# Kernel tuning notes

Hardware: AMD Instinct MI355X
Metric: run time of the kernel (lower is better)

The kernel has to match this reference:

```python
import jax, jax.numpy as jnp
import numpy as np

SPOT_DIM = 512
PROTEIN_DIM = 512
NUM_CLASSES = 32
NUM_PROTEINS = 64
BATCH = 4096
INPUT_DIM = SPOT_DIM + NUM_CLASSES          # 544
H1 = INPUT_DIM // 4                          # 136
H2 = INPUT_DIM // 2                          # 272


def leaky_relu(x, slope=0.2):
    return jnp.where(x > 0, x, slope * x)


def setup_inputs() -> dict:
    key = jax.random.key(0)
    ks = jax.random.split(key, 13)
    s = 0.02
    return {
        "cell_embeddings_protein": jax.random.normal(ks[0], (BATCH, SPOT_DIM), jnp.float32),
        "cond_label": jax.random.normal(ks[1], (BATCH, NUM_CLASSES), jnp.float32),
        "protein_emb": jax.random.normal(ks[2], (BATCH, NUM_PROTEINS, PROTEIN_DIM), jnp.float32),
        # protein_projection: Linear(protein_dim -> spot_dim)
        "proj_W": jax.random.normal(ks[3], (PROTEIN_DIM, SPOT_DIM), jnp.float32) * s,
        "proj_b": jnp.zeros((SPOT_DIM,), jnp.float32),
        # trans_dim: Linear(input_dim + spot_dim -> input_dim)
        "trans_W": jax.random.normal(ks[4], (INPUT_DIM + SPOT_DIM, INPUT_DIM), jnp.float32) * s,
        "trans_b": jnp.zeros((INPUT_DIM,), jnp.float32),
        # per-protein 3-layer MLPs, stacked over proteins (grouped GEMM form)
        "W1": jax.random.normal(ks[5], (NUM_PROTEINS, INPUT_DIM, H1), jnp.float32) * s,
        "b1": jnp.zeros((NUM_PROTEINS, H1), jnp.float32),
        "W2": jax.random.normal(ks[6], (NUM_PROTEINS, H1, H2), jnp.float32) * s,
        "b2": jnp.zeros((NUM_PROTEINS, H2), jnp.float32),
        "W3": jax.random.normal(ks[7], (NUM_PROTEINS, H2, 1), jnp.float32) * s,
        "b3": jnp.zeros((NUM_PROTEINS, 1), jnp.float32),
    }


def reference(cell_embeddings_protein, cond_label, protein_emb,
              proj_W, proj_b, trans_W, trans_b,
              W1, b1, W2, b2, W3, b3):
    # [B, P, spot_dim]
    protein_projected = jnp.einsum("bpd,de->bpe", protein_emb, proj_W) + proj_b
    # [B, input_dim] -> broadcast to [B, P, input_dim]
    spot_encoded = jnp.concatenate([cell_embeddings_protein, cond_label], axis=-1)
    spot_encoded = jnp.broadcast_to(spot_encoded[:, None, :],
                                    (spot_encoded.shape[0], NUM_PROTEINS, INPUT_DIM))
    x = jnp.concatenate([protein_projected, spot_encoded], axis=-1)  # [B,P,1056]
    x = jnp.einsum("bpi,io->bpo", x, trans_W) + trans_b              # [B,P,544]
    # grouped per-protein MLP as batched matmuls over P
    h = leaky_relu(jnp.einsum("bpi,pij->bpj", x, W1) + b1)           # [B,P,136]
    h = leaky_relu(jnp.einsum("bpj,pjk->bpk", h, W2) + b2)           # [B,P,272]
    out = jnp.einsum("bpk,pko->bpo", h, W3) + b3                     # [B,P,1]
    return out[..., 0]                                               # [B,P]
```

## Files before the change

kernel.cpp:

```cpp
#include <hip/hip_runtime.h>


typedef short bf16x8 __attribute__((ext_vector_type(8)));
typedef unsigned short u16;
typedef u16 u16x8 __attribute__((ext_vector_type(8)));
typedef float f32x4 __attribute__((ext_vector_type(4)));

typedef const void __attribute__((address_space(1)))* gas_p;
typedef void __attribute__((address_space(3)))* las_p;

__device__ __forceinline__ void gl_lds16(const void* g, void* l) {
  __builtin_amdgcn_global_load_lds((gas_p)g, (las_p)l, 16, 0, 0);
}

__device__ __forceinline__ u16 f2bf(float f) {
  union { float f; unsigned u; } x; x.f = f;
  return (u16)((x.u + 0x7FFFu + ((x.u >> 16) & 1u)) >> 16);
}


__global__ __launch_bounds__(256)
void k_g(const float* __restrict__ projW, const float* __restrict__ transW,
         float* __restrict__ G) {
  __shared__ float As[16][68];
  __shared__ float Bs[16][68];
  const int t = threadIdx.x;
  const int m0 = blockIdx.x * 64, c0 = blockIdx.y * 64;
  const int tx = t & 15, ty = t >> 4;
  const int ar = t >> 2, akk = (t & 3) * 4;
  const int bkk = t >> 4, bcc = (t & 15) * 4;
  const bool bok = (c0 + bcc) < 544;
  float acc[4][4];
#pragma unroll
  for (int i = 0; i < 4; ++i)
#pragma unroll
    for (int j = 0; j < 4; ++j) acc[i][j] = 0.f;

  for (int k0 = 0; k0 < 512; k0 += 16) {
    const float4 av = *(const float4*)(projW + (size_t)(m0 + ar) * 512 + k0 + akk);
    float4 bv = {0.f, 0.f, 0.f, 0.f};
    if (bok) bv = *(const float4*)(transW + (size_t)(k0 + bkk) * 544 + c0 + bcc);
    __syncthreads();
    As[akk + 0][ar] = av.x; As[akk + 1][ar] = av.y;
    As[akk + 2][ar] = av.z; As[akk + 3][ar] = av.w;
    *(float4*)&Bs[bkk][bcc] = bv;
    __syncthreads();
#pragma unroll
    for (int kk = 0; kk < 16; ++kk) {
      const float4 a = *(const float4*)&As[kk][ty * 4];
      const float4 b = *(const float4*)&Bs[kk][tx * 4];
      const float aa[4] = {a.x, a.y, a.z, a.w};
      const float bb[4] = {b.x, b.y, b.z, b.w};
#pragma unroll
      for (int i = 0; i < 4; ++i)
#pragma unroll
        for (int j = 0; j < 4; ++j) acc[i][j] += aa[i] * bb[j];
    }
  }
  if ((c0 + tx * 4) < 544) {
#pragma unroll
    for (int i = 0; i < 4; ++i) {
      float4 v = {acc[i][0], acc[i][1], acc[i][2], acc[i][3]};
      *(float4*)(G + (size_t)(m0 + ty * 4 + i) * 544 + c0 + tx * 4) = v;
    }
  }
}

__global__ void k_gcopy(const float* __restrict__ transW, float* __restrict__ G) {
  const int idx = blockIdx.x * 256 + threadIdx.x;
  if (idx >= 73984) return;
  ((float4*)G)[69632 + idx] = ((const float4*)transW)[69632 + idx];
}

__global__ void k_d(const float* __restrict__ projb, const float* __restrict__ transW,
                    const float* __restrict__ transb, float* __restrict__ dvec) {
  __shared__ float red[256];
  const int t = threadIdx.x;
  const int c = blockIdx.x * 32 + (t & 31);
  const int kp = t >> 5;
  float s = 0.f;
  for (int k = kp * 64; k < kp * 64 + 64; ++k) s += projb[k] * transW[(size_t)k * 544 + c];
  red[t] = s;
  __syncthreads();
  if (t < 32) {
    float v = red[t];
#pragma unroll
    for (int j = 1; j < 8; ++j) v += red[t + 32 * j];
    dvec[blockIdx.x * 32 + t] = v + transb[blockIdx.x * 32 + t];
  }
}

__global__ void k_c(const float* __restrict__ dvec, const float* __restrict__ W1,
                    const float* __restrict__ b1, float* __restrict__ cvec) {
  __shared__ float red[256];
  const int t = threadIdx.x;
  const int p = blockIdx.x, cg = blockIdx.y;
  const int col = cg * 16 + (t & 15);
  const int kp = t >> 4;
  float s = 0.f;
  if (col < 136) {
    const float* w = W1 + (size_t)p * 544 * 136;
    for (int k = kp * 34; k < kp * 34 + 34; ++k) s += dvec[k] * w[(size_t)k * 136 + col];
  }
  red[t] = s;
  __syncthreads();
  if (t < 16) {
    float v = 0.f;
#pragma unroll
    for (int j = 0; j < 16; ++j) v += red[j * 16 + t];
    const int c2 = cg * 16 + t;
    cvec[p * 144 + c2] = (c2 < 136) ? v + b1[p * 136 + c2] : 0.f;
  }
}

__global__ void k_pack_w1(const float* __restrict__ W1, u16* __restrict__ W1pk) {
  const int uid = blockIdx.x * 256 + threadIdx.x;
  const int unit = uid & 63;
  const int rest = uid >> 6;
  const int n = rest % 9;
  const int tile = rest / 9;
  const int kt = tile % 17;
  const int pp = tile / 17;
  const int kb = unit >> 4, cl = unit & 15;
  const int colg = n * 16 + cl;
  u16x8 v;
#pragma unroll
  for (int j = 0; j < 8; ++j) {
    const int k = kt * 32 + kb * 8 + j;
    v[j] = (colg < 136) ? f2bf(W1[((size_t)pp * 544 + k) * 136 + colg]) : (u16)0;
  }
  *(u16x8*)(W1pk + (size_t)uid * 8) = v;
}

__global__ void k_pack_w2(const float* __restrict__ W2, u16* __restrict__ W2pk) {
  const int uid = blockIdx.x * 256 + threadIdx.x;
  const int unit = uid & 63;
  const int rest = uid >> 6;
  const int n = rest % 17;
  const int tile = rest / 17;
  const int kt = tile % 5;
  const int pp = tile / 5;
  const int kb = unit >> 4, cl = unit & 15;
  const int colg = n * 16 + cl;
  u16x8 v;
#pragma unroll
  for (int j = 0; j < 8; ++j) {
    const int k = kt * 32 + kb * 8 + j;
    v[j] = (k < 136) ? f2bf(W2[((size_t)pp * 136 + k) * 272 + colg]) : (u16)0;
  }
  *(u16x8*)(W2pk + (size_t)uid * 8) = v;
}

__global__ __launch_bounds__(256, 2)
void k_pk3(const float* __restrict__ G, const u16* __restrict__ W1pk,
           u16* __restrict__ Wpk) {
  __shared__ char smem[34816];
  char* const Ab0 = smem;
  char* const Bb0 = smem + 16384;
  const int t = threadIdx.x, lane = t & 63, w = t >> 6;
  const int l15 = lane & 15, kq = lane >> 4;
  const int mt = blockIdx.x, p = blockIdx.y;
  const int sr = t >> 1, sh = t & 1, sf = (sr >> 1) & 3;
  const int gr = mt * 128 + sr;
  const bool aval = (gr < 1056);

  const f32x4 fz = {0.f, 0.f, 0.f, 0.f};
  f32x4 acc[2][9];
#pragma unroll
  for (int m = 0; m < 2; ++m)
#pragma unroll
    for (int n = 0; n < 9; ++n) acc[m][n] = fz;

  const u16* wsrc = W1pk + (size_t)p * (17 * 4608);

  float4 pv[4];
  auto preloadA = [&](int kt) {
    if (aval) {
      const float* s = G + (size_t)gr * 544 + kt * 32 + sh * 16;
#pragma unroll
      for (int j = 0; j < 4; ++j) pv[j] = *(const float4*)(s + j * 4);
    } else {
      const float4 z4 = {0.f, 0.f, 0.f, 0.f};
#pragma unroll
      for (int j = 0; j < 4; ++j) pv[j] = z4;
    }
  };
  auto writeA = [&](int buf) {
    u16x8 v0, v1;
    v0[0] = f2bf(pv[0].x); v0[1] = f2bf(pv[0].y); v0[2] = f2bf(pv[0].z); v0[3] = f2bf(pv[0].w);
    v0[4] = f2bf(pv[1].x); v0[5] = f2bf(pv[1].y); v0[6] = f2bf(pv[1].z); v0[7] = f2bf(pv[1].w);
    v1[0] = f2bf(pv[2].x); v1[1] = f2bf(pv[2].y); v1[2] = f2bf(pv[2].z); v1[3] = f2bf(pv[2].w);
    v1[4] = f2bf(pv[3].x); v1[5] = f2bf(pv[3].y); v1[6] = f2bf(pv[3].z); v1[7] = f2bf(pv[3].w);
    char* dst = Ab0 + buf * 8192 + sr * 64;
    *(u16x8*)(dst + ((((sh << 1)) ^ sf) << 4)) = v0;
    *(u16x8*)(dst + ((((sh << 1) | 1) ^ sf) << 4)) = v1;
  };
  auto stageB = [&](int kt, int buf) {
    const u16* src = wsrc + kt * 4608;
    char* dst = Bb0 + buf * 9216;
    for (int i = w; i < 9; i += 4) gl_lds16(src + i * 512 + lane * 8, dst + i * 1024);
  };
  auto compute = [&](int buf) {
    const char* A = Ab0 + buf * 8192;
    const char* Bt = Bb0 + buf * 9216;
    bf16x8 a[2];
#pragma unroll
    for (int m = 0; m < 2; ++m) {
      const int row = w * 32 + m * 16 + l15;
      a[m] = *(const bf16x8*)(A + row * 64 + ((kq ^ ((row >> 1) & 3)) << 4));
    }
#pragma unroll
    for (int n = 0; n < 9; ++n) {
      bf16x8 b = *(const bf16x8*)(Bt + n * 1024 + lane * 16);
      acc[0][n] = __builtin_amdgcn_mfma_f32_16x16x32_bf16(a[0], b, acc[0][n], 0, 0, 0);
      acc[1][n] = __builtin_amdgcn_mfma_f32_16x16x32_bf16(a[1], b, acc[1][n], 0, 0, 0);
    }
  };

  preloadA(0); stageB(0, 0); writeA(0);
  for (int kt = 0; kt < 17; ++kt) {
    __syncthreads();
    const int buf = kt & 1;
    if (kt + 1 < 17) { preloadA(kt + 1); stageB(kt + 1, buf ^ 1); }
    compute(buf);
    if (kt + 1 < 17) writeA(buf ^ 1);
  }

#pragma unroll
  for (int m = 0; m < 2; ++m)
#pragma unroll
    for (int n = 0; n < 9; ++n)
#pragma unroll
      for (int i = 0; i < 4; ++i) {
        const int row = mt * 128 + w * 32 + m * 16 + (kq << 2) + i;
        if (row < 1056) {
          const int ktw = row >> 5, kk = row & 31;
          const size_t off = (size_t)(p * 33 + ktw) * 4608 + n * 512 +
                             ((kk >> 3) * 16 + l15) * 8 + (kk & 7);
          Wpk[off] = f2bf(acc[m][n][i]);
        }
      }
}

__global__ __launch_bounds__(256, 2)
void k_main(const float* __restrict__ cell, const float* __restrict__ cond,
            const float* __restrict__ pe,
            const u16* __restrict__ Wpk, const u16* __restrict__ W2pk,
            const float* __restrict__ cvec, const float* __restrict__ b2,
            const float* __restrict__ W3, const float* __restrict__ b3,
            float* __restrict__ out) {
  __shared__ char smem[58368];
  char* const Ab0 = smem;
  char* const Bb0 = smem + 16384;
  char* const h1  = smem + 17408;
  char* const B2  = smem;

  const int t = threadIdx.x, lane = t & 63, w = t >> 6;
  const int l15 = lane & 15, kq = lane >> 4;
  const int p = blockIdx.y;
  const int b0 = blockIdx.x * 128;
  const int sr = t >> 1, sh = t & 1, sf = (sr >> 1) & 3;
  const long gr = b0 + sr;

  const f32x4 fz = {0.f, 0.f, 0.f, 0.f};
  f32x4 acc[2][9];
#pragma unroll
  for (int m = 0; m < 2; ++m)
#pragma unroll
    for (int n = 0; n < 9; ++n) acc[m][n] = fz;

  const u16* wsrc = Wpk + (size_t)p * (33 * 4608);

  float4 pv[4];
  auto preloadA = [&](int kt) {
    const float* s;
    if (kt < 16)      s = pe + ((gr * 64 + p) << 9) + kt * 32 + sh * 16;
    else if (kt < 32) s = cell + (gr << 9) + (kt - 16) * 32 + sh * 16;
    else              s = cond + (gr << 5) + sh * 16;
#pragma unroll
    for (int j = 0; j < 4; ++j) pv[j] = *(const float4*)(s + j * 4);
  };
  auto writeA = [&](int buf) {
    u16x8 v0, v1;
    v0[0] = f2bf(pv[0].x); v0[1] = f2bf(pv[0].y); v0[2] = f2bf(pv[0].z); v0[3] = f2bf(pv[0].w);
    v0[4] = f2bf(pv[1].x); v0[5] = f2bf(pv[1].y); v0[6] = f2bf(pv[1].z); v0[7] = f2bf(pv[1].w);
    v1[0] = f2bf(pv[2].x); v1[1] = f2bf(pv[2].y); v1[2] = f2bf(pv[2].z); v1[3] = f2bf(pv[2].w);
    v1[4] = f2bf(pv[3].x); v1[5] = f2bf(pv[3].y); v1[6] = f2bf(pv[3].z); v1[7] = f2bf(pv[3].w);
    char* dst = Ab0 + buf * 8192 + sr * 64;
    *(u16x8*)(dst + ((((sh << 1)) ^ sf) << 4)) = v0;
    *(u16x8*)(dst + ((((sh << 1) | 1) ^ sf) << 4)) = v1;
  };
  auto stageB = [&](int kt, int buf) {
    const u16* src = wsrc + kt * 4608;
    char* dst = Bb0 + buf * 9216;
    for (int i = w; i < 9; i += 4) gl_lds16(src + i * 512 + lane * 8, dst + i * 1024);
  };
  auto compute1 = [&](int buf) {
    const char* A = Ab0 + buf * 8192;
    const char* Bt = Bb0 + buf * 9216;
    bf16x8 a[2];
#pragma unroll
    for (int m = 0; m < 2; ++m) {
      const int row = w * 32 + m * 16 + l15;
      a[m] = *(const bf16x8*)(A + row * 64 + ((kq ^ ((row >> 1) & 3)) << 4));
    }
#pragma unroll
    for (int n = 0; n < 9; ++n) {
      bf16x8 b = *(const bf16x8*)(Bt + n * 1024 + lane * 16);
      acc[0][n] = __builtin_amdgcn_mfma_f32_16x16x32_bf16(a[0], b, acc[0][n], 0, 0, 0);
      acc[1][n] = __builtin_amdgcn_mfma_f32_16x16x32_bf16(a[1], b, acc[1][n], 0, 0, 0);
    }
  };

  preloadA(0); stageB(0, 0); writeA(0);
  for (int kt = 0; kt < 33; ++kt) {
    __syncthreads();
    const int buf = kt & 1;
    if (kt + 1 < 33) { preloadA(kt + 1); stageB(kt + 1, buf ^ 1); }
    compute1(buf);
    if (kt + 1 < 33) writeA(buf ^ 1);
  }
  __syncthreads();

  {
    const float* cp = cvec + p * 144;
#pragma unroll
    for (int m = 0; m < 2; ++m) {
      const int rb = w * 32 + m * 16 + (kq << 2);
#pragma unroll
      for (int n = 0; n < 9; ++n) {
        const int col = n * 16 + l15;
        const float cb = cp[col];
#pragma unroll
        for (int i = 0; i < 4; ++i) {
          const int row = rb + i;
          float v = acc[m][n][i] + cb;
          v = v > 0.f ? v : 0.2f * v;
          const int u = (col >> 3) ^ ((row >> 1) & 3);
          *(u16*)(h1 + row * 320 + u * 16 + ((col & 7) << 1)) = f2bf(v);
        }
      }
    }
    const int uz = (18 + sh) ^ sf;
    u16x8 z = {0, 0, 0, 0, 0, 0, 0, 0};
    *(u16x8*)(h1 + sr * 320 + uz * 16) = z;
  }

  f32x4 acc2[2][17];
#pragma unroll
  for (int m = 0; m < 2; ++m)
#pragma unroll
    for (int n = 0; n < 17; ++n) acc2[m][n] = fz;

  const u16* w2src = W2pk + (size_t)p * (5 * 8704);
  for (int kt = 0; kt < 5; ++kt) {
    for (int i = w; i < 17; i += 4)
      gl_lds16(w2src + kt * 8704 + i * 512 + lane * 8, B2 + i * 1024);
    __syncthreads();
    bf16x8 a[2];
#pragma unroll
    for (int m = 0; m < 2; ++m) {
      const int row = w * 32 + m * 16 + l15;
      const int u = (kt * 4 + kq) ^ ((row >> 1) & 3);
      a[m] = *(const bf16x8*)(h1 + row * 320 + u * 16);
    }
#pragma unroll
    for (int n = 0; n < 17; ++n) {
      bf16x8 b = *(const bf16x8*)(B2 + n * 1024 + lane * 16);
      acc2[0][n] = __builtin_amdgcn_mfma_f32_16x16x32_bf16(a[0], b, acc2[0][n], 0, 0, 0);
      acc2[1][n] = __builtin_amdgcn_mfma_f32_16x16x32_bf16(a[1], b, acc2[1][n], 0, 0, 0);
    }
    __syncthreads();
  }

  {
    const float* w3p = W3 + p * 272;
    const float* b2p = b2 + p * 272;
    const float b3v = b3[p];
    float w3v[17], b2v[17];
#pragma unroll
    for (int n = 0; n < 17; ++n) { w3v[n] = w3p[n * 16 + l15]; b2v[n] = b2p[n * 16 + l15]; }
#pragma unroll
    for (int m = 0; m < 2; ++m) {
#pragma unroll
      for (int i = 0; i < 4; ++i) {
        float s = 0.f;
#pragma unroll
        for (int n = 0; n < 17; ++n) {
          float h = acc2[m][n][i] + b2v[n];
          h = h > 0.f ? h : 0.2f * h;
          s += h * w3v[n];
        }
        s += __shfl_xor(s, 1);
        s += __shfl_xor(s, 2);
        s += __shfl_xor(s, 4);
        s += __shfl_xor(s, 8);
        if (l15 == 0) {
          const int row = w * 32 + m * 16 + (kq << 2) + i;
          out[(size_t)(b0 + row) * 64 + p] = s + b3v;
        }
      }
    }
  }
}

extern "C" void kernel_launch(void* const* d_in, const int* in_sizes, int n_in,
                              void* d_out, int out_size, void* d_ws, size_t ws_size,
                              hipStream_t stream) {
  const float* cell   = (const float*)d_in[0];
  const float* cond   = (const float*)d_in[1];
  const float* pe     = (const float*)d_in[2];
  const float* projW  = (const float*)d_in[3];
  const float* projb  = (const float*)d_in[4];
  const float* transW = (const float*)d_in[5];
  const float* transb = (const float*)d_in[6];
  const float* W1     = (const float*)d_in[7];
  const float* b1     = (const float*)d_in[8];
  const float* W2     = (const float*)d_in[9];
  const float* b2     = (const float*)d_in[10];
  const float* W3     = (const float*)d_in[11];
  const float* b3     = (const float*)d_in[12];
  float* out = (float*)d_out;

  char* ws = (char*)d_ws;
  float* G    = (float*)(ws);
  u16*  W1pk  = (u16*)(ws + 2297856);
  u16*  Wpk   = (u16*)(ws + 12324864);
  u16*  W2pk  = (u16*)(ws + 31789056);
  float* dvec = (float*)(ws + 37359616);
  float* cvec = (float*)(ws + 37361792);

  k_g      <<<dim3(8, 9),   256, 0, stream>>>(projW, transW, G);
  k_gcopy  <<<289,  256, 0, stream>>>(transW, G);
  k_d      <<<17,   256, 0, stream>>>(projb, transW, transb, dvec);
  k_c      <<<dim3(64, 9),  256, 0, stream>>>(dvec, W1, b1, cvec);
  k_pack_w1<<<2448, 256, 0, stream>>>(W1, W1pk);
  k_pack_w2<<<1360, 256, 0, stream>>>(W2, W2pk);
  k_pk3    <<<dim3(9, 64),  256, 0, stream>>>(G, W1pk, Wpk);
  k_main   <<<dim3(32, 64), 256, 0, stream>>>(cell, cond, pe, Wpk, W2pk, cvec, b2, W3, b3, out);
}
```

Baseline: 328.9 us.

## Merge preprocessing kernels, fold bias GEMV into pk3, retile main to 2x2 waves

Six small preprocessing launches become one k_pre kernel that dispatches on block index. The bias vector d is written as an extra row of G, so k_pk3 produces cvec as a byproduct and k_d and k_c go away. Both MFMA kernels change their wave tiling from 4x1 to 2x2, giving each wave 64 rows by up to 5 column tiles to raise A and B register reuse. k_main also gets a swizzled 1D block-to-protein mapping for cache locality and a larger LDS layout. The larger LDS footprint and accumulator count may lower occupancy.

```diff
diff --git a/kernel.cpp b/kernel.cpp
--- a/kernel.cpp
+++ b/kernel.cpp
@@ -18,172 +18,146 @@
   return (u16)((x.u + 0x7FFFu + ((x.u >> 16) & 1u)) >> 16);
 }
 
-
 __global__ __launch_bounds__(256)
-void k_g(const float* __restrict__ projW, const float* __restrict__ transW,
-         float* __restrict__ G) {
+void k_pre(const float* __restrict__ projW, const float* __restrict__ transW,
+           const float* __restrict__ projb, const float* __restrict__ transb,
+           const float* __restrict__ W1, const float* __restrict__ W2,
+           float* __restrict__ G, u16* __restrict__ W1pk, u16* __restrict__ W2pk) {
   __shared__ float As[16][68];
   __shared__ float Bs[16][68];
-  const int t = threadIdx.x;
-  const int m0 = blockIdx.x * 64, c0 = blockIdx.y * 64;
-  const int tx = t & 15, ty = t >> 4;
-  const int ar = t >> 2, akk = (t & 3) * 4;
-  const int bkk = t >> 4, bcc = (t & 15) * 4;
-  const bool bok = (c0 + bcc) < 544;
-  float acc[4][4];
-#pragma unroll
-  for (int i = 0; i < 4; ++i)
-#pragma unroll
-    for (int j = 0; j < 4; ++j) acc[i][j] = 0.f;
-
-  for (int k0 = 0; k0 < 512; k0 += 16) {
-    const float4 av = *(const float4*)(projW + (size_t)(m0 + ar) * 512 + k0 + akk);
-    float4 bv = {0.f, 0.f, 0.f, 0.f};
-    if (bok) bv = *(const float4*)(transW + (size_t)(k0 + bkk) * 544 + c0 + bcc);
+  const int bb = blockIdx.x, t = threadIdx.x;
+
+  if (bb < 72) {
+    const int m0 = (bb & 7) * 64, c0 = (bb >> 3) * 64;
+    const int tx = t & 15, ty = t >> 4;
+    const int ar = t >> 2, akk = (t & 3) * 4;
+    const int bkk = t >> 4, bcc = (t & 15) * 4;
+    const bool bok = (c0 + bcc) < 544;
+    float acc[4][4];
+#pragma unroll
+    for (int i = 0; i < 4; ++i)
+#pragma unroll
+      for (int j = 0; j < 4; ++j) acc[i][j] = 0.f;
+    for (int k0 = 0; k0 < 512; k0 += 16) {
+      const float4 av = *(const float4*)(projW + (size_t)(m0 + ar) * 512 + k0 + akk);
+      float4 bv = {0.f, 0.f, 0.f, 0.f};
+      if (bok) bv = *(const float4*)(transW + (size_t)(k0 + bkk) * 544 + c0 + bcc);
+      __syncthreads();
+      As[akk + 0][ar] = av.x; As[akk + 1][ar] = av.y;
+      As[akk + 2][ar] = av.z; As[akk + 3][ar] = av.w;
+      *(float4*)&Bs[bkk][bcc] = bv;
+      __syncthreads();
+#pragma unroll
+      for (int kk = 0; kk < 16; ++kk) {
+        const float4 a = *(const float4*)&As[kk][ty * 4];
+        const float4 b = *(const float4*)&Bs[kk][tx * 4];
+        const float aa[4] = {a.x, a.y, a.z, a.w};
+        const float bb2[4] = {b.x, b.y, b.z, b.w};
+#pragma unroll
+        for (int i = 0; i < 4; ++i)
+#pragma unroll
+          for (int j = 0; j < 4; ++j) acc[i][j] += aa[i] * bb2[j];
+      }
+    }
+    if ((c0 + tx * 4) < 544) {
+#pragma unroll
+      for (int i = 0; i < 4; ++i) {
+        float4 v = {acc[i][0], acc[i][1], acc[i][2], acc[i][3]};
+        *(float4*)(G + (size_t)(m0 + ty * 4 + i) * 544 + c0 + tx * 4) = v;
+      }
+    }
+  } else if (bb < 361) {
+    const int idx = (bb - 72) * 256 + t;
+    if (idx < 73984) ((float4*)G)[69632 + idx] = ((const float4*)transW)[69632 + idx];
+  } else if (bb < 378) {
+    __shared__ float red[256];
+    const int c = (bb - 361) * 32 + (t & 31);
+    const int kp = t >> 5;
+    float s = 0.f;
+    for (int k = kp * 64; k < kp * 64 + 64; ++k) s += projb[k] * transW[(size_t)k * 544 + c];
+    red[t] = s;
     __syncthreads();
-    As[akk + 0][ar] = av.x; As[akk + 1][ar] = av.y;
-    As[akk + 2][ar] = av.z; As[akk + 3][ar] = av.w;
-    *(float4*)&Bs[bkk][bcc] = bv;
-    __syncthreads();
-#pragma unroll
-    for (int kk = 0; kk < 16; ++kk) {
-      const float4 a = *(const float4*)&As[kk][ty * 4];
-      const float4 b = *(const float4*)&Bs[kk][tx * 4];
-      const float aa[4] = {a.x, a.y, a.z, a.w};
-      const float bb[4] = {b.x, b.y, b.z, b.w};
-#pragma unroll
-      for (int i = 0; i < 4; ++i)
-#pragma unroll
-        for (int j = 0; j < 4; ++j) acc[i][j] += aa[i] * bb[j];
-    }
-  }
-  if ((c0 + tx * 4) < 544) {
-#pragma unroll
-    for (int i = 0; i < 4; ++i) {
-      float4 v = {acc[i][0], acc[i][1], acc[i][2], acc[i][3]};
-      *(float4*)(G + (size_t)(m0 + ty * 4 + i) * 544 + c0 + tx * 4) = v;
-    }
-  }
-}
-
-__global__ void k_gcopy(const float* __restrict__ transW, float* __restrict__ G) {
-  const int idx = blockIdx.x * 256 + threadIdx.x;
-  if (idx >= 73984) return;
-  ((float4*)G)[69632 + idx] = ((const float4*)transW)[69632 + idx];
-}
-
-__global__ void k_d(const float* __restrict__ projb, const float* __restrict__ transW,
-                    const float* __restrict__ transb, float* __restrict__ dvec) {
-  __shared__ float red[256];
-  const int t = threadIdx.x;
-  const int c = blockIdx.x * 32 + (t & 31);
-  const int kp = t >> 5;
-  float s = 0.f;
-  for (int k = kp * 64; k < kp * 64 + 64; ++k) s += projb[k] * transW[(size_t)k * 544 + c];
-  red[t] = s;
-  __syncthreads();
-  if (t < 32) {
-    float v = red[t];
-#pragma unroll
-    for (int j = 1; j < 8; ++j) v += red[t + 32 * j];
-    dvec[blockIdx.x * 32 + t] = v + transb[blockIdx.x * 32 + t];
-  }
-}
-
-__global__ void k_c(const float* __restrict__ dvec, const float* __restrict__ W1,
-                    const float* __restrict__ b1, float* __restrict__ cvec) {
-  __shared__ float red[256];
-  const int t = threadIdx.x;
-  const int p = blockIdx.x, cg = blockIdx.y;
-  const int col = cg * 16 + (t & 15);
-  const int kp = t >> 4;
-  float s = 0.f;
-  if (col < 136) {
-    const float* w = W1 + (size_t)p * 544 * 136;
-    for (int k = kp * 34; k < kp * 34 + 34; ++k) s += dvec[k] * w[(size_t)k * 136 + col];
-  }
-  red[t] = s;
-  __syncthreads();
-  if (t < 16) {
-    float v = 0.f;
-#pragma unroll
-    for (int j = 0; j < 16; ++j) v += red[j * 16 + t];
-    const int c2 = cg * 16 + t;
-    cvec[p * 144 + c2] = (c2 < 136) ? v + b1[p * 136 + c2] : 0.f;
-  }
-}
-
-__global__ void k_pack_w1(const float* __restrict__ W1, u16* __restrict__ W1pk) {
-  const int uid = blockIdx.x * 256 + threadIdx.x;
-  const int unit = uid & 63;
-  const int rest = uid >> 6;
-  const int n = rest % 9;
-  const int tile = rest / 9;
-  const int kt = tile % 17;
-  const int pp = tile / 17;
-  const int kb = unit >> 4, cl = unit & 15;
-  const int colg = n * 16 + cl;
-  u16x8 v;
-#pragma unroll
-  for (int j = 0; j < 8; ++j) {
-    const int k = kt * 32 + kb * 8 + j;
-    v[j] = (colg < 136) ? f2bf(W1[((size_t)pp * 544 + k) * 136 + colg]) : (u16)0;
-  }
-  *(u16x8*)(W1pk + (size_t)uid * 8) = v;
-}
-
-__global__ void k_pack_w2(const float* __restrict__ W2, u16* __restrict__ W2pk) {
-  const int uid = blockIdx.x * 256 + threadIdx.x;
-  const int unit = uid & 63;
-  const int rest = uid >> 6;
-  const int n = rest % 17;
-  const int tile = rest / 17;
-  const int kt = tile % 5;
-  const int pp = tile / 5;
-  const int kb = unit >> 4, cl = unit & 15;
-  const int colg = n * 16 + cl;
-  u16x8 v;
-#pragma unroll
-  for (int j = 0; j < 8; ++j) {
-    const int k = kt * 32 + kb * 8 + j;
-    v[j] = (k < 136) ? f2bf(W2[((size_t)pp * 136 + k) * 272 + colg]) : (u16)0;
-  }
-  *(u16x8*)(W2pk + (size_t)uid * 8) = v;
+    if (t < 32) {
+      float v = red[t];
+#pragma unroll
+      for (int j = 1; j < 8; ++j) v += red[t + 32 * j];
+      const int cc = (bb - 361) * 32 + t;
+      G[(size_t)1056 * 544 + cc] = v + transb[cc];
+    }
+  } else if (bb < 391) {
+    const int idx = (bb - 378) * 256 + t;
+    const float4 z = {0.f, 0.f, 0.f, 0.f};
+#pragma unroll
+    for (int j = 0; j < 4; ++j) {
+      const int k = idx + j * 3328;
+      if (k < 12920) ((float4*)G)[143752 + k] = z;
+    }
+  } else if (bb < 2839) {
+    const int uid = (bb - 391) * 256 + t;
+    const int unit = uid & 63;
+    const int rest = uid >> 6;
+    const int n = rest % 9;
+    const int tile = rest / 9;
+    const int kt = tile % 17;
+    const int pp = tile / 17;
+    const int kb = unit >> 4, cl = unit & 15;
+    const int colg = n * 16 + cl;
+    u16x8 v;
+#pragma unroll
+    for (int j = 0; j < 8; ++j) {
+      const int k = kt * 32 + kb * 8 + j;
+      v[j] = (colg < 136) ? f2bf(W1[((size_t)pp * 544 + k) * 136 + colg]) : (u16)0;
+    }
+    *(u16x8*)(W1pk + (size_t)uid * 8) = v;
+  } else {
+    const int uid = (bb - 2839) * 256 + t;
+    const int unit = uid & 63;
+    const int rest = uid >> 6;
+    const int n = rest % 17;
+    const int tile = rest / 17;
+    const int kt = tile % 5;
+    const int pp = tile / 5;
+    const int kb = unit >> 4, cl = unit & 15;
+    const int colg = n * 16 + cl;
+    u16x8 v;
+#pragma unroll
+    for (int j = 0; j < 8; ++j) {
+      const int k = kt * 32 + kb * 8 + j;
+      v[j] = (k < 136) ? f2bf(W2[((size_t)pp * 136 + k) * 272 + colg]) : (u16)0;
+    }
+    *(u16x8*)(W2pk + (size_t)uid * 8) = v;
+  }
 }
 
 __global__ __launch_bounds__(256, 2)
 void k_pk3(const float* __restrict__ G, const u16* __restrict__ W1pk,
-           u16* __restrict__ Wpk) {
+           const float* __restrict__ b1, u16* __restrict__ Wpk,
+           float* __restrict__ cvec) {
   __shared__ char smem[34816];
   char* const Ab0 = smem;
   char* const Bb0 = smem + 16384;
   const int t = threadIdx.x, lane = t & 63, w = t >> 6;
   const int l15 = lane & 15, kq = lane >> 4;
+  const int mg = w >> 1, ng = w & 1;
+  const int n0 = ng * 5, nn = ng ? 4 : 5;
   const int mt = blockIdx.x, p = blockIdx.y;
   const int sr = t >> 1, sh = t & 1, sf = (sr >> 1) & 3;
   const int gr = mt * 128 + sr;
-  const bool aval = (gr < 1056);
 
   const f32x4 fz = {0.f, 0.f, 0.f, 0.f};
-  f32x4 acc[2][9];
-#pragma unroll
-  for (int m = 0; m < 2; ++m)
-#pragma unroll
-    for (int n = 0; n < 9; ++n) acc[m][n] = fz;
+  f32x4 acc[4][5];
+#pragma unroll
+  for (int m = 0; m < 4; ++m)
+#pragma unroll
+    for (int n = 0; n < 5; ++n) acc[m][n] = fz;
 
   const u16* wsrc = W1pk + (size_t)p * (17 * 4608);
 
   float4 pv[4];
   auto preloadA = [&](int kt) {
-    if (aval) {
-      const float* s = G + (size_t)gr * 544 + kt * 32 + sh * 16;
-#pragma unroll
-      for (int j = 0; j < 4; ++j) pv[j] = *(const float4*)(s + j * 4);
-    } else {
-      const float4 z4 = {0.f, 0.f, 0.f, 0.f};
-#pragma unroll
-      for (int j = 0; j < 4; ++j) pv[j] = z4;
-    }
+    const float* s = G + (size_t)gr * 544 + kt * 32 + sh * 16;
+#pragma unroll
+    for (int j = 0; j < 4; ++j) pv[j] = *(const float4*)(s + j * 4);
   };
   auto writeA = [&](int buf) {
     u16x8 v0, v1;
@@ -203,17 +177,20 @@
   auto compute = [&](int buf) {
     const char* A = Ab0 + buf * 8192;
     const char* Bt = Bb0 + buf * 9216;
-    bf16x8 a[2];
-#pragma unroll
-    for (int m = 0; m < 2; ++m) {
-      const int row = w * 32 + m * 16 + l15;
+    bf16x8 a[4];
+#pragma unroll
+    for (int m = 0; m < 4; ++m) {
+      const int row = mg * 64 + m * 16 + l15;
       a[m] = *(const bf16x8*)(A + row * 64 + ((kq ^ ((row >> 1) & 3)) << 4));
     }
 #pragma unroll
-    for (int n = 0; n < 9; ++n) {
-      bf16x8 b = *(const bf16x8*)(Bt + n * 1024 + lane * 16);
-      acc[0][n] = __builtin_amdgcn_mfma_f32_16x16x32_bf16(a[0], b, acc[0][n], 0, 0, 0);
-      acc[1][n] = __builtin_amdgcn_mfma_f32_16x16x32_bf16(a[1], b, acc[1][n], 0, 0, 0);
+    for (int n = 0; n < 5; ++n) {
+      if (n < nn) {
+        bf16x8 b = *(const bf16x8*)(Bt + (n0 + n) * 1024 + lane * 16);
+#pragma unroll
+        for (int m = 0; m < 4; ++m)
+          acc[m][n] = __builtin_amdgcn_mfma_f32_16x16x32_bf16(a[m], b, acc[m][n], 0, 0, 0);
+      }
     }
   };
 
@@ -227,19 +204,25 @@
   }
 
 #pragma unroll
-  for (int m = 0; m < 2; ++m)
-#pragma unroll
-    for (int n = 0; n < 9; ++n)
-#pragma unroll
-      for (int i = 0; i < 4; ++i) {
-        const int row = mt * 128 + w * 32 + m * 16 + (kq << 2) + i;
-        if (row < 1056) {
-          const int ktw = row >> 5, kk = row & 31;
-          const size_t off = (size_t)(p * 33 + ktw) * 4608 + n * 512 +
-                             ((kk >> 3) * 16 + l15) * 8 + (kk & 7);
-          Wpk[off] = f2bf(acc[m][n][i]);
+  for (int m = 0; m < 4; ++m)
+#pragma unroll
+    for (int n = 0; n < 5; ++n) {
+      if (n < nn) {
+#pragma unroll
+        for (int i = 0; i < 4; ++i) {
+          const int row = mt * 128 + mg * 64 + m * 16 + (kq << 2) + i;
+          const int col = (n0 + n) * 16 + l15;
+          if (row < 1056) {
+            const int ktw = row >> 5, kk = row & 31;
+            const size_t off = (size_t)(p * 33 + ktw) * 4608 + (n0 + n) * 512 +
+                               ((kk >> 3) * 16 + l15) * 8 + (kk & 7);
+            Wpk[off] = f2bf(acc[m][n][i]);
+          } else if (row == 1056) {
+            cvec[p * 144 + col] = (col < 136) ? acc[m][n][i] + b1[p * 136 + col] : 0.f;
+          }
         }
       }
+    }
 }
 
 __global__ __launch_bounds__(256, 2)
@@ -249,25 +232,30 @@
             const float* __restrict__ cvec, const float* __restrict__ b2,
             const float* __restrict__ W3, const float* __restrict__ b3,
             float* __restrict__ out) {
-  __shared__ char smem[58368];
-  char* const Ab0 = smem;
-  char* const Bb0 = smem + 16384;
-  char* const h1  = smem + 17408;
-  char* const B2  = smem;
+  __shared__ char smem[75776];
+  char* const h1  = smem;
+  char* const Ab0 = smem + 40960;
+  char* const Bb0 = smem + 57344;
+  char* const B2  = smem + 40960;
 
   const int t = threadIdx.x, lane = t & 63, w = t >> 6;
   const int l15 = lane & 15, kq = lane >> 4;
-  const int p = blockIdx.y;
-  const int b0 = blockIdx.x * 128;
+  const int mg = w >> 1, ng = w & 1;
+  const int n0 = ng * 5, nn = ng ? 4 : 5;
+
+  const unsigned lid = blockIdx.x;
+  const int p  = ((lid & 7) << 3) | ((lid >> 8) & 7);
+  const int b0 = ((lid >> 3) & 31) * 128;
+
   const int sr = t >> 1, sh = t & 1, sf = (sr >> 1) & 3;
   const long gr = b0 + sr;
 
   const f32x4 fz = {0.f, 0.f, 0.f, 0.f};
-  f32x4 acc[2][9];
-#pragma unroll
-  for (int m = 0; m < 2; ++m)
-#pragma unroll
-    for (int n = 0; n < 9; ++n) acc[m][n] = fz;
+  f32x4 acc[4][5];
+#pragma unroll
+  for (int m = 0; m < 4; ++m)
+#pragma unroll
+    for (int n = 0; n < 5; ++n) acc[m][n] = fz;
 
   const u16* wsrc = Wpk + (size_t)p * (33 * 4608);
 
@@ -298,17 +286,20 @@
   auto compute1 = [&](int buf) {
     const char* A = Ab0 + buf * 8192;
     const char* Bt = Bb0 + buf * 9216;
-    bf16x8 a[2];
-#pragma unroll
-    for (int m = 0; m < 2; ++m) {
-      const int row = w * 32 + m * 16 + l15;
+    bf16x8 a[4];
+#pragma unroll
+    for (int m = 0; m < 4; ++m) {
+      const int row = mg * 64 + m * 16 + l15;
       a[m] = *(const bf16x8*)(A + row * 64 + ((kq ^ ((row >> 1) & 3)) << 4));
     }
 #pragma unroll
-    for (int n = 0; n < 9; ++n) {
-      bf16x8 b = *(const bf16x8*)(Bt + n * 1024 + lane * 16);
-      acc[0][n] = __builtin_amdgcn_mfma_f32_16x16x32_bf16(a[0], b, acc[0][n], 0, 0, 0);
-      acc[1][n] = __builtin_amdgcn_mfma_f32_16x16x32_bf16(a[1], b, acc[1][n], 0, 0, 0);
+    for (int n = 0; n < 5; ++n) {
+      if (n < nn) {
+        bf16x8 b = *(const bf16x8*)(Bt + (n0 + n) * 1024 + lane * 16);
+#pragma unroll
+        for (int m = 0; m < 4; ++m)
+          acc[m][n] = __builtin_amdgcn_mfma_f32_16x16x32_bf16(a[m], b, acc[m][n], 0, 0, 0);
+      }
     }
   };
 
@@ -325,19 +316,21 @@
   {
     const float* cp = cvec + p * 144;
 #pragma unroll
-    for (int m = 0; m < 2; ++m) {
-      const int rb = w * 32 + m * 16 + (kq << 2);
-#pragma unroll
-      for (int n = 0; n < 9; ++n) {
-        const int col = n * 16 + l15;
-        const float cb = cp[col];
-#pragma unroll
-        for (int i = 0; i < 4; ++i) {
-          const int row = rb + i;
-          float v = acc[m][n][i] + cb;
-          v = v > 0.f ? v : 0.2f * v;
-          const int u = (col >> 3) ^ ((row >> 1) & 3);
-          *(u16*)(h1 + row * 320 + u * 16 + ((col & 7) << 1)) = f2bf(v);
+    for (int m = 0; m < 4; ++m) {
+      const int rb = mg * 64 + m * 16 + (kq << 2);
+#pragma unroll
+      for (int n = 0; n < 5; ++n) {
+        if (n < nn) {
+          const int col = (n0 + n) * 16 + l15;
+          const float cb = cp[col];
+#pragma unroll
+          for (int i = 0; i < 4; ++i) {
+            const int row = rb + i;
+            float v = acc[m][n][i] + cb;
+            v = v > 0.f ? v : 0.2f * v;
+            const int u = (col >> 3) ^ ((row >> 1) & 3);
+            *(u16*)(h1 + row * 320 + u * 16 + ((col & 7) << 1)) = f2bf(v);
+          }
         }
       }
     }
@@ -345,6 +338,7 @@
     u16x8 z = {0, 0, 0, 0, 0, 0, 0, 0};
     *(u16x8*)(h1 + sr * 320 + uz * 16) = z;
   }
+  __syncthreads();
 
   f32x4 acc2[2][17];
 #pragma unroll
@@ -424,18 +418,12 @@
 
   char* ws = (char*)d_ws;
   float* G    = (float*)(ws);
-  u16*  W1pk  = (u16*)(ws + 2297856);
-  u16*  Wpk   = (u16*)(ws + 12324864);
-  u16*  W2pk  = (u16*)(ws + 31789056);
-  float* dvec = (float*)(ws + 37359616);
-  float* cvec = (float*)(ws + 37361792);
-
-  k_g      <<<dim3(8, 9),   256, 0, stream>>>(projW, transW, G);
-  k_gcopy  <<<289,  256, 0, stream>>>(transW, G);
-  k_d      <<<17,   256, 0, stream>>>(projb, transW, transb, dvec);
-  k_c      <<<dim3(64, 9),  256, 0, stream>>>(dvec, W1, b1, cvec);
-  k_pack_w1<<<2448, 256, 0, stream>>>(W1, W1pk);
-  k_pack_w2<<<1360, 256, 0, stream>>>(W2, W2pk);
-  k_pk3    <<<dim3(9, 64),  256, 0, stream>>>(G, W1pk, Wpk);
-  k_main   <<<dim3(32, 64), 256, 0, stream>>>(cell, cond, pe, Wpk, W2pk, cvec, b2, W3, b3, out);
-}
+  u16*  W1pk  = (u16*)(ws + 2506752);
+  u16*  Wpk   = (u16*)(ws + 12533760);
+  u16*  W2pk  = (u16*)(ws + 31997952);
+  float* cvec = (float*)(ws + 37568512);
+
+  k_pre <<<4199, 256, 0, stream>>>(projW, transW, projb, transb, W1, W2, G, W1pk, W2pk);
+  k_pk3 <<<dim3(9, 64), 256, 0, stream>>>(G, W1pk, b1, Wpk, cvec);
+  k_main<<<2048, 256, 0, stream>>>(cell, cond, pe, Wpk, W2pk, cvec, b2, W3, b3, out);
+}
```

After: 326.4 us. Within noise of the previous version (-0.8%).
